# Kernel optimization log

Measured on AMD Instinct MI355X. Metric: run time of the kernel, lower is better.

Reference implementation:

```python
import jax, jax.numpy as jnp
import numpy as np

B, T, I, D = 16, 128, 8, 128


def layer_norm(x, g, b, eps=1e-5):
    mu = jnp.mean(x, -1, keepdims=True)
    var = jnp.mean((x - mu) ** 2, -1, keepdims=True)
    return (x - mu) * jax.lax.rsqrt(var + eps) * g + b


def setup_inputs() -> dict:
    key = jax.random.key(0)
    ks = jax.random.split(key, 8)
    vectors = jax.random.normal(ks[0], (B, T, T, I), jnp.float32)
    # structured pairwise mask: mask[b,i,j] = real[b,i] & real[b,j]
    lengths = jax.random.randint(ks[1], (B,), T // 2, T + 1)
    real = jnp.arange(T)[None, :] < lengths[:, None]  # [B,T]
    mask = real[:, :, None] & real[:, None, :]  # [B,T,T]
    s = lambda n: 1.0 / np.sqrt(n)
    W_embed = jax.random.normal(ks[2], (I, D), jnp.float32) * s(I)
    b_embed = jnp.zeros((D,), jnp.float32)
    ln1_g = jnp.ones((D,), jnp.float32)
    ln1_b = jnp.zeros((D,), jnp.float32)
    Wq = jax.random.normal(ks[3], (D, D), jnp.float32) * s(D)
    Wk = jax.random.normal(ks[4], (D, D), jnp.float32) * s(D)
    Wv = jax.random.normal(ks[5], (D, D), jnp.float32) * s(D)
    W_out = jax.random.normal(ks[6], (D, D), jnp.float32) * s(D)
    b_out = jnp.zeros((D,), jnp.float32)
    ln2_g = jnp.ones((D,), jnp.float32)
    ln2_b = jnp.zeros((D,), jnp.float32)
    return dict(vectors=vectors, mask=mask, W_embed=W_embed, b_embed=b_embed,
                ln1_g=ln1_g, ln1_b=ln1_b, Wq=Wq, Wk=Wk, Wv=Wv,
                W_out=W_out, b_out=b_out, ln2_g=ln2_g, ln2_b=ln2_b)


def reference(vectors, mask, W_embed, b_embed, ln1_g, ln1_b, Wq, Wk, Wv,
              W_out, b_out, ln2_g, ln2_b):
    Bs, Tn = vectors.shape[0], vectors.shape[1]
    Dm = W_embed.shape[1]
    square_mask = jnp.transpose(mask, (1, 2, 0))            # [T,T,B] bool
    seq = square_mask[jnp.arange(Tn), jnp.arange(Tn)]       # [T,B] bool (diagonal)
    # shared embedding stack (masked) + norm, on flattened [T*T,B,*]
    x = jnp.transpose(vectors.reshape(Bs, Tn * Tn, -1), (1, 0, 2))  # [T*T,B,I]
    mflat = square_mask.reshape(Tn * Tn, Bs, 1).astype(x.dtype)
    x = jax.nn.gelu(x @ W_embed + b_embed) * mflat
    x = layer_norm(x, ln1_g, ln1_b)
    x = x.reshape(Tn, Tn, Bs, Dm)                           # [T,T,B,D]
    keys = x @ Wk                                            # [T,T,B,D]
    values = x @ Wv                                          # [T,T,B,D]
    queries = x[jnp.arange(Tn), jnp.arange(Tn)] @ Wq         # diag gather -> [T,B,D]
    # attention mask: pairwise-real OR self
    amask = square_mask | jnp.eye(Tn, dtype=bool)[:, :, None]  # [T,T,B]
    logits = jnp.einsum('rbd,rcbd->rcb', queries, keys) / np.sqrt(Dm)
    logits = logits + jnp.where(amask, 0.0, -1e9)
    w = jax.nn.softmax(logits, axis=1)                       # [T,T,B]
    emb = jnp.einsum('rcb,rcbd->rbd', w, values)             # [T,B,D]
    # output linear block with skip connection, masked by sequence mask
    seq_f = seq[:, :, None].astype(emb.dtype)                # [T,B,1]
    h = jax.nn.gelu(emb @ W_out + b_out)
    embeddings = layer_norm(h + emb, ln2_g, ln2_b) * seq_f   # [T,B,D]
    padding_mask = ~jnp.transpose(seq)                       # [B,T]
    sequence_mask = seq[:, :, None]                          # [T,B,1]
    global_mask = jnp.ones((Tn,), dtype=bool)                # [T]
    return embeddings, padding_mask, sequence_mask, global_mask
```

## Files before the change

### kernel.cpp

```cpp
#include <hip/hip_runtime.h>
#include <hip/hip_fp16.h>
#include <math.h>

#define BB 16
#define TT 128
#define II 8
#define DD 128
#define SCALE 0.08838834764831845f

#define WS_WVO_OFF 16384
#define WS_LEN_OFF 32768


__device__ __forceinline__ float sgelu(float x) {
    float x2 = x * x;
    float w = x * (-1.5957691216f - 0.07135481627f * x2);
    float e = __expf(w);
    return __fdividef(x, 1.0f + e);
}

__device__ __forceinline__ float fast_gelu(float x) {
    float u = 1.5957691216057308f * x * (1.0f + 0.044715f * x * x);
    float e = __expf(u);
    float th = 1.0f - __fdividef(2.0f, e + 1.0f);
    return 0.5f * x * (1.0f + th);
}

__global__ void k0_setup(const float* __restrict__ Wq,
                         const float* __restrict__ Wk,
                         const float* __restrict__ Wv,
                         const float* __restrict__ Wo,
                         const int* __restrict__ mask,
                         float* __restrict__ M,
                         float* __restrict__ WvWo,
                         int* __restrict__ lens) {
    int blk = blockIdx.x;
    if (blk == DD) {
        __shared__ int cnt[BB];
        int t = threadIdx.x;
        if (t < BB) cnt[t] = 0;
        __syncthreads();
        for (int b = 0; b < BB; b++) {
            if (mask[b * TT * TT + t * TT + t]) atomicAdd(&cnt[b], 1);
        }
        __syncthreads();
        if (t < BB) lens[t] = cnt[t];
        return;
    }
    __shared__ float row[DD];
    int d = threadIdx.x;
    if (blk < DD) {
        int a = blk;
        row[d] = Wq[a * DD + d];
        __syncthreads();
        const float4* wk4 = (const float4*)(Wk + d * DD);
        float acc = 0.0f;
        #pragma unroll 8
        for (int e4 = 0; e4 < DD / 4; e4++) {
            float4 w = wk4[e4];
            acc += row[e4 * 4 + 0] * w.x + row[e4 * 4 + 1] * w.y +
                   row[e4 * 4 + 2] * w.z + row[e4 * 4 + 3] * w.w;
        }
        M[a * DD + d] = acc;
    } else {
        int a = blk - DD - 1;
        row[d] = Wv[a * DD + d];
        __syncthreads();
        float acc = 0.0f;
        #pragma unroll 8
        for (int e = 0; e < DD; e++) acc += row[e] * Wo[e * DD + d];
        WvWo[a * DD + d] = acc;
    }
}

__global__ __launch_bounds__(256, 4)
void k_main(const float* __restrict__ vectors,
            const int* __restrict__ lens,
            const float* __restrict__ We,
            const float* __restrict__ be,
            const float* __restrict__ g1,
            const float* __restrict__ b1,
            const float* __restrict__ M,
            const float* __restrict__ Wv,
            const float* __restrict__ WvWo,
            const float* __restrict__ bo,
            const float* __restrict__ g2,
            const float* __restrict__ b2,
            float* __restrict__ out) {
    __shared__ __half2 xsh[TT * 64];
    __shared__ float  xrs[DD];
    __shared__ float  kqs[DD];
    __shared__ float  lgt[TT];
    __shared__ float  wgt[TT];
    __shared__ float2 pbuf[256];
    __shared__ float2 sv2[64];

    int n = blockIdx.x;
    int b = n >> 7, r = n & 127;
    int t = threadIdx.x, wave = t >> 6, lane = t & 63;
    int hh = lane >> 5, sl = lane & 31;
    int dl = sl * 4;
    int len = lens[b];

    if (r >= len) {
        if (wave == 0) {
            int rb_out = r * BB + b;
            ((float2*)out)[rb_out * 64 + lane] = make_float2(0.0f, 0.0f);
            if (lane == 0) {
                out[262144 + b * TT + r] = 1.0f;
                out[264192 + r * BB + b] = 0.0f;
                if (b == 0) out[266240 + r] = 1.0f;
            }
        }
        return;
    }

    const float4* vb4 = (const float4*)(vectors + (size_t)n * TT * II);

    float4 we4[II];
    #pragma unroll
    for (int i = 0; i < II; i++) we4[i] = *(const float4*)(We + i * DD + dl);
    float4 be4 = *(const float4*)(be + dl);
    float4 g14 = *(const float4*)(g1 + dl);
    float4 b14 = *(const float4*)(b1 + dl);

    {
        float4 v0 = vb4[2 * r], v1 = vb4[2 * r + 1];
        float vv[8] = {v0.x, v0.y, v0.z, v0.w, v1.x, v1.y, v1.z, v1.w};
        float e0 = be4.x, e1 = be4.y, e2 = be4.z, e3 = be4.w;
        #pragma unroll
        for (int i = 0; i < II; i++) {
            e0 += vv[i] * we4[i].x; e1 += vv[i] * we4[i].y;
            e2 += vv[i] * we4[i].z; e3 += vv[i] * we4[i].w;
        }
        float a0 = sgelu(e0), a1 = sgelu(e1), a2 = sgelu(e2), a3 = sgelu(e3);
        float s = (a0 + a1) + (a2 + a3);
        float q = (a0 * a0 + a1 * a1) + (a2 * a2 + a3 * a3);
        #pragma unroll
        for (int o = 16; o >= 1; o >>= 1) {
            s += __shfl_xor(s, o, 64); q += __shfl_xor(q, o, 64);
        }
        float mu = s * (1.0f / 128.0f);
        float rstd = rsqrtf(q * (1.0f / 128.0f) - mu * mu + 1e-5f);
        float x0 = (a0 - mu) * rstd * g14.x + b14.x;
        float x1 = (a1 - mu) * rstd * g14.y + b14.y;
        float x2 = (a2 - mu) * rstd * g14.z + b14.z;
        float x3 = (a3 - mu) * rstd * g14.w + b14.w;
        if (t < 32) ((float4*)xrs)[sl] = make_float4(x0, x1, x2, x3);
    }
    __syncthreads();

    {
        const float2* M2 = (const float2*)M;
        float ax = 0.0f, ay = 0.0f;
        #pragma unroll 8
        for (int j = 0; j < 32; j++) {
            int a = (wave << 5) + j;
            float xv = xrs[a];
            float2 m2 = M2[a * 64 + lane];
            ax += xv * m2.x; ay += xv * m2.y;
        }
        pbuf[t] = make_float2(ax, ay);
    }
    __syncthreads();
    if (t < 64) {
        float2 p0 = pbuf[t], p1 = pbuf[64 + t], p2 = pbuf[128 + t], p3 = pbuf[192 + t];
        kqs[2 * t]     = (p0.x + p1.x + p2.x + p3.x) * SCALE;
        kqs[2 * t + 1] = (p0.y + p1.y + p2.y + p3.y) * SCALE;
    }
    __syncthreads();

    float4 kq4 = *(const float4*)&kqs[dl];
    float4 u4 = make_float4(g14.x * kq4.x, g14.y * kq4.y, g14.z * kq4.z, g14.w * kq4.w);
    float Us, C0;
    {
        float us = (u4.x + u4.y) + (u4.z + u4.w);
        float c0 = (b14.x * kq4.x + b14.y * kq4.y) + (b14.z * kq4.z + b14.w * kq4.w);
        #pragma unroll
        for (int o = 16; o >= 1; o >>= 1) {
            us += __shfl_xor(us, o, 64); c0 += __shfl_xor(c0, o, 64);
        }
        Us = us; C0 = c0;
    }

    {
        int g = (wave << 1) + hh;
        int jmax = (len - g + 15) >> 4;
        for (int j = 0; j < jmax; j++) {
            int cA = (j << 4) + g;
            int cB = cA + 8;
            float4 vA0 = vb4[2 * cA], vA1 = vb4[2 * cA + 1];
            float4 vB0 = vb4[2 * cB], vB1 = vb4[2 * cB + 1];
            float vA[8] = {vA0.x, vA0.y, vA0.z, vA0.w, vA1.x, vA1.y, vA1.z, vA1.w};
            float vB[8] = {vB0.x, vB0.y, vB0.z, vB0.w, vB1.x, vB1.y, vB1.z, vB1.w};
            float eA0 = be4.x, eA1 = be4.y, eA2 = be4.z, eA3 = be4.w;
            float eB0 = be4.x, eB1 = be4.y, eB2 = be4.z, eB3 = be4.w;
            #pragma unroll
            for (int i = 0; i < II; i++) {
                eA0 += vA[i] * we4[i].x; eA1 += vA[i] * we4[i].y;
                eA2 += vA[i] * we4[i].z; eA3 += vA[i] * we4[i].w;
                eB0 += vB[i] * we4[i].x; eB1 += vB[i] * we4[i].y;
                eB2 += vB[i] * we4[i].z; eB3 += vB[i] * we4[i].w;
            }
            float aA0 = sgelu(eA0), aA1 = sgelu(eA1), aA2 = sgelu(eA2), aA3 = sgelu(eA3);
            float aB0 = sgelu(eB0), aB1 = sgelu(eB1), aB2 = sgelu(eB2), aB3 = sgelu(eB3);
            float sA = (aA0 + aA1) + (aA2 + aA3);
            float qA = (aA0 * aA0 + aA1 * aA1) + (aA2 * aA2 + aA3 * aA3);
            float pA = (aA0 * u4.x + aA1 * u4.y) + (aA2 * u4.z + aA3 * u4.w);
            float sB = (aB0 + aB1) + (aB2 + aB3);
            float qB = (aB0 * aB0 + aB1 * aB1) + (aB2 * aB2 + aB3 * aB3);
            float pB = (aB0 * u4.x + aB1 * u4.y) + (aB2 * u4.z + aB3 * u4.w);
            #pragma unroll
            for (int o = 16; o >= 1; o >>= 1) {
                sA += __shfl_xor(sA, o, 64); qA += __shfl_xor(qA, o, 64);
                pA += __shfl_xor(pA, o, 64);
                sB += __shfl_xor(sB, o, 64); qB += __shfl_xor(qB, o, 64);
                pB += __shfl_xor(pB, o, 64);
            }
            float muA = sA * (1.0f / 128.0f), muB = sB * (1.0f / 128.0f);
            float rsA = rsqrtf(qA * (1.0f / 128.0f) - muA * muA + 1e-5f);
            float rsB = rsqrtf(qB * (1.0f / 128.0f) - muB * muB + 1e-5f);
            float xA0 = (aA0 - muA) * rsA * g14.x + b14.x;
            float xA1 = (aA1 - muA) * rsA * g14.y + b14.y;
            float xA2 = (aA2 - muA) * rsA * g14.z + b14.z;
            float xA3 = (aA3 - muA) * rsA * g14.w + b14.w;
            float xB0 = (aB0 - muB) * rsB * g14.x + b14.x;
            float xB1 = (aB1 - muB) * rsB * g14.y + b14.y;
            float xB2 = (aB2 - muB) * rsB * g14.z + b14.z;
            float xB3 = (aB3 - muB) * rsB * g14.w + b14.w;
            {
                __half2 p0 = __floats2half2_rn(xA0, xA1), p1 = __floats2half2_rn(xA2, xA3);
                uint2 st; st.x = *(unsigned*)&p0; st.y = *(unsigned*)&p1;
                ((uint2*)(xsh + cA * 64))[sl] = st;
                if (sl == 0) lgt[cA] = rsA * (pA - muA * Us) + C0;
            }
            if (cB < len) {
                __half2 p0 = __floats2half2_rn(xB0, xB1), p1 = __floats2half2_rn(xB2, xB3);
                uint2 st; st.x = *(unsigned*)&p0; st.y = *(unsigned*)&p1;
                ((uint2*)(xsh + cB * 64))[sl] = st;
                if (sl == 0) lgt[cB] = rsB * (pB - muB * Us) + C0;
            }
        }
    }
    __syncthreads();

    if (wave == 0) {
        float l0 = lgt[lane];
        float l1 = (lane + 64 < len) ? lgt[lane + 64] : -1e9f;
        float mx = fmaxf(l0, l1);
        #pragma unroll
        for (int o = 32; o >= 1; o >>= 1) mx = fmaxf(mx, __shfl_xor(mx, o, 64));
        float e0 = __expf(l0 - mx), e1 = __expf(l1 - mx);
        float s = e0 + e1;
        #pragma unroll
        for (int o = 32; o >= 1; o >>= 1) s += __shfl_xor(s, o, 64);
        float inv = __fdividef(1.0f, s);
        wgt[lane] = e0 * inv; wgt[lane + 64] = e1 * inv;
    }
    __syncthreads();

    {
        int jw = (len - wave + 3) >> 2;
        float ax = 0.0f, ay = 0.0f;
        for (int j = 0; j < jw; j++) {
            int c = (j << 2) + wave;
            float w = wgt[c];
            float2 xf = __half22float2(xsh[c * 64 + lane]);
            ax += w * xf.x; ay += w * xf.y;
        }
        pbuf[t] = make_float2(ax, ay);
    }
    __syncthreads();
    if (t < 64) {
        float2 p0 = pbuf[t], p1 = pbuf[64 + t], p2 = pbuf[128 + t], p3 = pbuf[192 + t];
        sv2[t] = make_float2(p0.x + p1.x + p2.x + p3.x, p0.y + p1.y + p2.y + p3.y);
    }
    __syncthreads();

    {
        const float* svf = (const float*)sv2;
        const float2* W2 = (wave < 2) ? (const float2*)Wv : (const float2*)WvWo;
        int abase = (wave & 1) << 6;
        float ax = 0.0f, ay = 0.0f;
        #pragma unroll 8
        for (int j = 0; j < 64; j++) {
            int a = abase + j;
            float s = svf[a];
            float2 w2 = W2[a * 64 + lane];
            ax += s * w2.x; ay += s * w2.y;
        }
        pbuf[t] = make_float2(ax, ay);
    }
    __syncthreads();

    if (wave == 0) {
        float2 e0 = pbuf[lane], e1 = pbuf[64 + lane];
        float2 h0p = pbuf[128 + lane], h1p = pbuf[192 + lane];
        float2 bo2 = ((const float2*)bo)[lane];
        float em0 = e0.x + e1.x, em1 = e0.y + e1.y;
        float h0 = fast_gelu(h0p.x + h1p.x + bo2.x);
        float h1 = fast_gelu(h0p.y + h1p.y + bo2.y);
        float z0 = h0 + em0, z1 = h1 + em1;
        float s = z0 + z1, q = z0 * z0 + z1 * z1;
        #pragma unroll
        for (int o = 32; o >= 1; o >>= 1) {
            s += __shfl_xor(s, o, 64); q += __shfl_xor(q, o, 64);
        }
        float mu = s * (1.0f / 128.0f);
        float rstd = rsqrtf(q * (1.0f / 128.0f) - mu * mu + 1e-5f);
        float2 g22 = ((const float2*)g2)[lane], b22 = ((const float2*)b2)[lane];
        float u0 = z0 - mu, u1 = z1 - mu;
        int rb_out = r * BB + b;
        ((float2*)out)[rb_out * 64 + lane] =
            make_float2(u0 * rstd * g22.x + b22.x,
                        u1 * rstd * g22.y + b22.y);
        if (lane == 0) {
            out[262144 + b * TT + r] = 0.0f;
            out[264192 + r * BB + b] = 1.0f;
            if (b == 0) out[266240 + r] = 1.0f;
        }
    }
}

extern "C" void kernel_launch(void* const* d_in, const int* in_sizes, int n_in,
                              void* d_out, int out_size, void* d_ws, size_t ws_size,
                              hipStream_t stream) {
    const float* vectors = (const float*)d_in[0];
    const int*   mask    = (const int*)d_in[1];
    const float* W_embed = (const float*)d_in[2];
    const float* b_embed = (const float*)d_in[3];
    const float* ln1_g   = (const float*)d_in[4];
    const float* ln1_b   = (const float*)d_in[5];
    const float* Wq      = (const float*)d_in[6];
    const float* Wk      = (const float*)d_in[7];
    const float* Wv      = (const float*)d_in[8];
    const float* W_out   = (const float*)d_in[9];
    const float* b_out   = (const float*)d_in[10];
    const float* ln2_g   = (const float*)d_in[11];
    const float* ln2_b   = (const float*)d_in[12];
    float* out = (float*)d_out;

    float* M    = (float*)d_ws;
    float* WvWo = (float*)d_ws + WS_WVO_OFF;
    int*   lens = (int*)((float*)d_ws + WS_LEN_OFF);

    hipLaunchKernelGGL(k0_setup, dim3(2 * DD + 1), dim3(DD), 0, stream,
                       Wq, Wk, Wv, W_out, mask, M, WvWo, lens);
    hipLaunchKernelGGL(k_main, dim3(TT * BB), dim3(256), 0, stream,
                       vectors, lens, W_embed, b_embed, ln1_g, ln1_b, M,
                       Wv, WvWo, b_out, ln2_g, ln2_b, out);
}
```

Baseline: 135.8 us.

## Keep normalized pair embeddings in registers and fuse softmax-weighted sum

The per-column layer-normed embeddings are now held as half2 values in registers, fully unrolled over eight iterations, instead of being written to a 32KB shared-memory tile. Every wave computes the softmax redundantly and fetches weights by shuffle, then accumulates the weighted sum straight from registers. Each wave also keeps its own copy of the diagonal row, which removes several __syncthreads and the kq reduction pass. The gains should be less shared-memory traffic and fewer barriers, which may raise occupancy. The costs are higher register pressure and an odd NaN-guard expression added to xB1.

Measured after the change: 160.2 us. 17.9% more time.

```diff
diff --git a/kernel.cpp b/kernel.cpp
--- a/kernel.cpp
+++ b/kernel.cpp
@@ -87,13 +87,11 @@
             const float* __restrict__ g2,
             const float* __restrict__ b2,
             float* __restrict__ out) {
-    __shared__ __half2 xsh[TT * 64];
-    __shared__ float  xrs[DD];
-    __shared__ float  kqs[DD];
+    __shared__ float  xrw[4 * DD];
+    __shared__ float2 pbuf[256];
+    __shared__ float  pbufE[4 * DD];
     __shared__ float  lgt[TT];
-    __shared__ float  wgt[TT];
-    __shared__ float2 pbuf[256];
-    __shared__ float2 sv2[64];
+    __shared__ float  sfin[DD];
 
     int n = blockIdx.x;
     int b = n >> 7, r = n & 127;
@@ -146,31 +144,37 @@
         float x1 = (a1 - mu) * rstd * g14.y + b14.y;
         float x2 = (a2 - mu) * rstd * g14.z + b14.z;
         float x3 = (a3 - mu) * rstd * g14.w + b14.w;
-        if (t < 32) ((float4*)xrs)[sl] = make_float4(x0, x1, x2, x3);
-    }
-    __syncthreads();
+        if (lane < 32) ((float4*)(xrw + (wave << 7)))[sl] = make_float4(x0, x1, x2, x3);
+    }
 
     {
         const float2* M2 = (const float2*)M;
+        const float* xw = xrw + (wave << 7);
         float ax = 0.0f, ay = 0.0f;
         #pragma unroll 8
         for (int j = 0; j < 32; j++) {
             int a = (wave << 5) + j;
-            float xv = xrs[a];
+            float xv = xw[a];
             float2 m2 = M2[a * 64 + lane];
             ax += xv * m2.x; ay += xv * m2.y;
         }
         pbuf[t] = make_float2(ax, ay);
     }
     __syncthreads();
-    if (t < 64) {
-        float2 p0 = pbuf[t], p1 = pbuf[64 + t], p2 = pbuf[128 + t], p3 = pbuf[192 + t];
-        kqs[2 * t]     = (p0.x + p1.x + p2.x + p3.x) * SCALE;
-        kqs[2 * t + 1] = (p0.y + p1.y + p2.y + p3.y) * SCALE;
-    }
-    __syncthreads();
-
-    float4 kq4 = *(const float4*)&kqs[dl];
+
+    float4 kq4;
+    {
+        int cp = sl * 2;
+        float2 p00 = pbuf[cp],       p10 = pbuf[64 + cp],
+               p20 = pbuf[128 + cp], p30 = pbuf[192 + cp];
+        float2 p01 = pbuf[cp + 1],       p11 = pbuf[64 + cp + 1],
+               p21 = pbuf[128 + cp + 1], p31 = pbuf[192 + cp + 1];
+        kq4.x = (p00.x + p10.x + p20.x + p30.x) * SCALE;
+        kq4.y = (p00.y + p10.y + p20.y + p30.y) * SCALE;
+        kq4.z = (p01.x + p11.x + p21.x + p31.x) * SCALE;
+        kq4.w = (p01.y + p11.y + p21.y + p31.y) * SCALE;
+    }
+
     float4 u4 = make_float4(g14.x * kq4.x, g14.y * kq4.y, g14.z * kq4.z, g14.w * kq4.w);
     float Us, C0;
     {
@@ -183,11 +187,12 @@
         Us = us; C0 = c0;
     }
 
-    {
-        int g = (wave << 1) + hh;
-        int jmax = (len - g + 15) >> 4;
-        for (int j = 0; j < jmax; j++) {
-            int cA = (j << 4) + g;
+    int g = (wave << 1) + hh;
+    __half2 xa01[8], xa23[8], xb01[8], xb23[8];
+    #pragma unroll
+    for (int j = 0; j < 8; j++) {
+        int cA = (j << 4) + g;
+        if (cA < len) {
             int cB = cA + 8;
             float4 vA0 = vb4[2 * cA], vA1 = vb4[2 * cA + 1];
             float4 vB0 = vb4[2 * cB], vB1 = vb4[2 * cB + 1];
@@ -225,26 +230,23 @@
             float xA2 = (aA2 - muA) * rsA * g14.z + b14.z;
             float xA3 = (aA3 - muA) * rsA * g14.w + b14.w;
             float xB0 = (aB0 - muB) * rsB * g14.x + b14.x;
-            float xB1 = (aB1 - muB) * rsB * g14.y + b14.y;
+            float xB1 = (aB0 == aB0 ? (aB1 - muB) * rsB * g14.y + b14.y : 0.0f);
             float xB2 = (aB2 - muB) * rsB * g14.z + b14.z;
             float xB3 = (aB3 - muB) * rsB * g14.w + b14.w;
-            {
-                __half2 p0 = __floats2half2_rn(xA0, xA1), p1 = __floats2half2_rn(xA2, xA3);
-                uint2 st; st.x = *(unsigned*)&p0; st.y = *(unsigned*)&p1;
-                ((uint2*)(xsh + cA * 64))[sl] = st;
-                if (sl == 0) lgt[cA] = rsA * (pA - muA * Us) + C0;
-            }
-            if (cB < len) {
-                __half2 p0 = __floats2half2_rn(xB0, xB1), p1 = __floats2half2_rn(xB2, xB3);
-                uint2 st; st.x = *(unsigned*)&p0; st.y = *(unsigned*)&p1;
-                ((uint2*)(xsh + cB * 64))[sl] = st;
-                if (sl == 0) lgt[cB] = rsB * (pB - muB * Us) + C0;
-            }
-        }
-    }
-    __syncthreads();
-
-    if (wave == 0) {
+            xa01[j] = __floats2half2_rn(xA0, xA1);
+            xa23[j] = __floats2half2_rn(xA2, xA3);
+            xb01[j] = __floats2half2_rn(xB0, xB1);
+            xb23[j] = __floats2half2_rn(xB2, xB3);
+            if (sl == 0) {
+                lgt[cA] = rsA * (pA - muA * Us) + C0;
+                lgt[cB] = rsB * (pB - muB * Us) + C0;
+            }
+        }
+    }
+    __syncthreads();
+
+    float w0, w1;
+    {
         float l0 = lgt[lane];
         float l1 = (lane + 64 < len) ? lgt[lane + 64] : -1e9f;
         float mx = fmaxf(l0, l1);
@@ -255,37 +257,47 @@
         #pragma unroll
         for (int o = 32; o >= 1; o >>= 1) s += __shfl_xor(s, o, 64);
         float inv = __fdividef(1.0f, s);
-        wgt[lane] = e0 * inv; wgt[lane + 64] = e1 * inv;
-    }
-    __syncthreads();
-
-    {
-        int jw = (len - wave + 3) >> 2;
-        float ax = 0.0f, ay = 0.0f;
-        for (int j = 0; j < jw; j++) {
-            int c = (j << 2) + wave;
-            float w = wgt[c];
-            float2 xf = __half22float2(xsh[c * 64 + lane]);
-            ax += w * xf.x; ay += w * xf.y;
-        }
-        pbuf[t] = make_float2(ax, ay);
-    }
-    __syncthreads();
-    if (t < 64) {
-        float2 p0 = pbuf[t], p1 = pbuf[64 + t], p2 = pbuf[128 + t], p3 = pbuf[192 + t];
-        sv2[t] = make_float2(p0.x + p1.x + p2.x + p3.x, p0.y + p1.y + p2.y + p3.y);
-    }
-    __syncthreads();
-
-    {
-        const float* svf = (const float*)sv2;
+        w0 = e0 * inv; w1 = e1 * inv;
+    }
+
+    {
+        float4 acc = make_float4(0.0f, 0.0f, 0.0f, 0.0f);
+        #pragma unroll
+        for (int j = 0; j < 8; j++) {
+            int cA = (j << 4) + g, cB = cA + 8;
+            float wA = (j < 4) ? __shfl(w0, cA, 64) : __shfl(w1, cA - 64, 64);
+            float wB = (j < 4) ? __shfl(w0, cB, 64) : __shfl(w1, cB - 64, 64);
+            if (cA < len) {
+                float2 fa0 = __half22float2(xa01[j]);
+                float2 fa1 = __half22float2(xa23[j]);
+                float2 fb0 = __half22float2(xb01[j]);
+                float2 fb1 = __half22float2(xb23[j]);
+                acc.x += wA * fa0.x + wB * fb0.x;
+                acc.y += wA * fa0.y + wB * fb0.y;
+                acc.z += wA * fa1.x + wB * fb1.x;
+                acc.w += wA * fa1.y + wB * fb1.y;
+            }
+        }
+        acc.x += __shfl_xor(acc.x, 32, 64);
+        acc.y += __shfl_xor(acc.y, 32, 64);
+        acc.z += __shfl_xor(acc.z, 32, 64);
+        acc.w += __shfl_xor(acc.w, 32, 64);
+        if (lane < 32) ((float4*)(pbufE + (wave << 7)))[sl] = acc;
+    }
+    __syncthreads();
+    if (t < DD) {
+        sfin[t] = (pbufE[t] + pbufE[128 + t]) + (pbufE[256 + t] + pbufE[384 + t]);
+    }
+    __syncthreads();
+
+    {
         const float2* W2 = (wave < 2) ? (const float2*)Wv : (const float2*)WvWo;
         int abase = (wave & 1) << 6;
         float ax = 0.0f, ay = 0.0f;
         #pragma unroll 8
         for (int j = 0; j < 64; j++) {
             int a = abase + j;
-            float s = svf[a];
+            float s = sfin[a];
             float2 w2 = W2[a * 64 + lane];
             ax += s * w2.x; ay += s * w2.y;
         }
```
